# Kernel optimization log

Hardware: AMD Instinct MI355X
Metric: run time of the kernel (lower is better)

The kernel has to match this reference:

```python
import jax, jax.numpy as jnp
import numpy as np

B, L, D = 512, 200, 128
N_ITEMS = 50001
T_STEPS = 4
TAU = 2.0
STEP = 1
V_TH = 1.0
SG_ALPHA = 4.0  # spikingjelly default surrogate.Sigmoid alpha


@jax.custom_vjp
def spike(x):
    return (x >= 0.0).astype(x.dtype)

def _spike_fwd(x):
    return spike(x), x

def _spike_bwd(x, g):
    s = jax.nn.sigmoid(SG_ALPHA * x)
    return (g * SG_ALPHA * s * (1.0 - s),)

spike.defvjp(_spike_fwd, _spike_bwd)


def lif_multistep(x):
    """Multi-step LIF (hard reset to 0, detach_reset). x: [T, ...] -> spikes [T, ...]."""
    def step(v, xt):
        v = v + (xt - v) / TAU  # charge (v_reset = 0)
        s = spike(v - V_TH)
        v = v - jax.lax.stop_gradient(s) * v  # hard reset, detached spike
        return v, s
    v0 = jnp.zeros_like(x[0])
    _, spikes = jax.lax.scan(step, v0, x)
    return spikes


def layernorm(x, g, b, eps=1e-5):
    m = x.mean(-1, keepdims=True)
    v = x.var(-1, keepdims=True)
    return (x - m) / jnp.sqrt(v + eps) * g + b


def _build_session_graphs(rng):
    lens = rng.integers(50, L + 1, size=B)
    item_seq = np.zeros((B, L), dtype=np.int64)
    for b in range(B):
        item_seq[b, :lens[b]] = rng.integers(1, N_ITEMS, size=lens[b])
    alias = np.zeros((B, L), dtype=np.int64)
    items = np.zeros((B, L), dtype=np.int64)
    A = np.zeros((B, L, 2 * L), dtype=np.float32)
    for b in range(B):
        u = item_seq[b]
        node = np.unique(u)  # sorted
        items[b, :len(node)] = node
        alias[b] = np.searchsorted(node, u)
        uA = np.zeros((L, L), dtype=np.float32)
        for i in range(L - 1):
            if u[i + 1] == 0:
                break
            r = np.searchsorted(node, u[i])
            c = np.searchsorted(node, u[i + 1])
            uA[r, c] = 1.0
        sin = uA.sum(0); sin[sin == 0] = 1.0
        sout = uA.sum(1); sout[sout == 0] = 1.0
        A[b, :, :L] = (uA / sin).T          # u_A_in.T
        A[b, :, L:] = ((uA.T / sout)).T     # u_A_out.T
    mask = item_seq > 0
    return A, alias, items, mask, lens.astype(np.int64)


def setup_inputs() -> dict:
    rng = np.random.default_rng(0)
    A, alias, items, mask, lens = _build_session_graphs(rng)
    stdv = 1.0 / np.sqrt(D)
    key = jax.random.key(0)
    ks = jax.random.split(key, 24)
    u = lambda k, shape: jax.random.uniform(k, shape, jnp.float32, -stdv, stdv)
    item_emb = u(ks[0], (N_ITEMS, D)).at[0].set(0.0)  # padding_idx=0
    return {
        "A": jnp.asarray(A),
        "alias_inputs": jnp.asarray(alias),
        "items": jnp.asarray(items),
        "mask": jnp.asarray(mask),
        "item_seq_len": jnp.asarray(lens),
        "item_emb": item_emb,
        "W_in": u(ks[1], (D, D)), "b_in": u(ks[2], (D,)),
        "W_out": u(ks[3], (D, D)), "b_out": u(ks[4], (D,)),
        "w_ih": u(ks[5], (3 * D, 2 * D)), "w_hh": u(ks[6], (3 * D, D)),
        "b_ih": u(ks[7], (3 * D,)), "b_hh": u(ks[8], (3 * D,)),
        "b_iah": u(ks[9], (D,)), "b_ioh": u(ks[10], (D,)),
        "W1": u(ks[11], (D, D)), "W2": u(ks[12], (D, D)),
        "W3": u(ks[13], (1, D)), "Wt": u(ks[14], (D, 2 * D)),
        "g_q": u(ks[15], (D,)), "beta_q": u(ks[16], (D,)),
        "g_sh": u(ks[17], (2 * D,)), "beta_sh": u(ks[18], (2 * D,)),
    }


def _forward(A, alias_inputs, items, mask, item_seq_len, item_emb,
             W_in, b_in, W_out, b_out, w_ih, w_hh, b_ih, b_hh, b_iah, b_ioh,
             W1, W2, W3, Wt, g_q, beta_q, g_sh, beta_sh):
    hidden = item_emb[items]  # [B,L,D]
    for _ in range(STEP):
        ein = hidden @ W_in.T + b_in
        eout = hidden @ W_out.T + b_out
        input_in = jnp.einsum('bij,bjd->bid', A[:, :, :L], ein) + b_iah
        input_out = jnp.einsum('bij,bjd->bid', A[:, :, L:], eout) + b_ioh
        inputs = jnp.concatenate([input_in, input_out], axis=-1)  # [B,L,2D]
        gi = inputs @ w_ih.T + b_ih  # [B,L,3D]
        gh = hidden @ w_hh.T + b_hh
        i_r, i_i, i_n = jnp.split(gi, 3, axis=-1)
        h_r, h_i, h_n = jnp.split(gh, 3, axis=-1)
        r = jax.nn.sigmoid(i_r + h_r)
        z = jax.nn.sigmoid(i_i + h_i)
        n = jnp.tanh(i_n + r * h_n)
        hidden = (1.0 - z) * hidden + z * n
    seq_hidden = jnp.take_along_axis(hidden, alias_inputs[..., None], axis=1)  # [B,L,D]
    ht = jnp.take_along_axis(seq_hidden, (item_seq_len - 1)[:, None, None], axis=1)[:, 0]  # [B,D]
    Qb = (ht @ W1.T)[:, None, :] + seq_hidden @ W2.T  # [B,L,D]
    Q = jnp.broadcast_to(Qb[None], (T_STEPS, B, L, D))
    Qs = lif_multistep(layernorm(Q, g_q, beta_q))
    alpha = Qs @ W3.T  # [T,B,L,1]
    mf = mask.astype(alpha.dtype)
    a = jnp.sum(alpha * seq_hidden[None] * mf[None, :, :, None], axis=2)  # [T,B,D]
    ht_T = jnp.broadcast_to(ht[None], (T_STEPS, B, D))
    sh = jnp.concatenate([a, ht_T], axis=-1)  # [T,B,2D]
    sh = layernorm(lif_multistep(sh), g_sh, beta_sh)
    return (sh @ Wt.T).mean(0)  # [B,D]


def reference(A, alias_inputs, items, mask, item_seq_len, item_emb,
              W_in, b_in, W_out, b_out, w_ih, w_hh, b_ih, b_hh, b_iah, b_ioh,
              W1, W2, W3, Wt, g_q, beta_q, g_sh, beta_sh):
    return _forward(A, alias_inputs, items, mask, item_seq_len, item_emb,
                    W_in, b_in, W_out, b_out, w_ih, w_hh, b_ih, b_hh, b_iah, b_ioh,
                    W1, W2, W3, Wt, g_q, beta_q, g_sh, beta_sh)
```

## Files before the change

kernel.cpp:

```cpp
#include <hip/hip_runtime.h>
#include <hip/hip_bf16.h>
#include <cstdint>
#include <cstddef>

#define B_ 512
#define L_ 200
#define D_ 128
#define M_ (B_*L_)
#define T_ 4

typedef short bf16x8 __attribute__((ext_vector_type(8)));
typedef unsigned short u16x8 __attribute__((ext_vector_type(8)));
typedef float f32x4 __attribute__((ext_vector_type(4)));

__device__ __forceinline__ float bf2f(unsigned short u){
  union { unsigned int i; float f; } c; c.i = ((unsigned int)u)<<16; return c.f;
}
__device__ __forceinline__ unsigned short f2bf(float f){
  union { float f; unsigned int i; } c; c.f = f;
  unsigned int r = c.i + 0x7FFFu + ((c.i>>16)&1u);
  return (unsigned short)(r>>16);
}
__device__ __forceinline__ float wsum(float v){
  #pragma unroll
  for (int m=1;m<64;m<<=1) v += __shfl_xor(v, m, 64);
  return v;
}
__device__ __forceinline__ void gload_lds16(const void* g, void* l){
  __builtin_amdgcn_global_load_lds(
      (const __attribute__((address_space(1))) void*)g,
      (__attribute__((address_space(3))) void*)l, 16, 0, 0);
}

__global__ __launch_bounds__(256)
void gemm_bt(const unsigned short* __restrict__ A, int lda,
             const unsigned short* __restrict__ Bt, int ldb,
             const float* __restrict__ bias,
             unsigned short* __restrict__ C, int ldc, int K,
             const int* __restrict__ mlimit, const int* __restrict__ gidx)
{
  const int m0 = blockIdx.y * 128;
  const int Mv = mlimit ? *mlimit : (1<<30);
  if (m0 >= Mv) return;
  __shared__ __align__(16) short sAs[2][128*32];
  __shared__ __align__(16) short sBs[2][128*32];
  const int tid = threadIdx.x;
  const int n0 = blockIdx.x * 128;
  const int lane = tid & 63;
  const int w = tid >> 6;
  const int wr = (w>>1)*64, wc = (w&1)*64;

  f32x4 acc[4][4];
  #pragma unroll
  for (int i=0;i<4;i++)
    #pragma unroll
    for (int j=0;j<4;j++) acc[i][j] = (f32x4){0.f,0.f,0.f,0.f};

  const int c1 = tid, c2 = tid + 256;
  const int r1 = c1>>2, s1 = c1&3, k1 = ((s1 ^ ((r1>>1)&3))&3)<<3;
  const int r2 = c2>>2, s2 = c2&3, k2 = ((s2 ^ ((r2>>1)&3))&3)<<3;
  int ar1 = m0 + r1, ar2 = m0 + r2;
  if (gidx){ ar1 = (ar1 < Mv) ? gidx[ar1] : 0; ar2 = (ar2 < Mv) ? gidx[ar2] : 0; }
  const int fr = lane & 15;
  const int fq = lane >> 4;
  const int fk = ((fq ^ ((fr>>1)&3))&3)<<3;

  auto stage = [&](int t){
    const int buf = t & 1, ks = t << 5;
    gload_lds16(A  + (size_t)ar1*lda + ks + k1, sAs[buf] + (size_t)c1*8);
    gload_lds16(A  + (size_t)ar2*lda + ks + k2, sAs[buf] + (size_t)c2*8);
    gload_lds16(Bt + (size_t)(n0 + r1)*ldb + ks + k1, sBs[buf] + (size_t)c1*8);
    gload_lds16(Bt + (size_t)(n0 + r2)*ldb + ks + k2, sBs[buf] + (size_t)c2*8);
  };
  const int nT = K >> 5;
  stage(0);
  __syncthreads();
  for (int t=0; t<nT; ++t){
    if (t+1 < nT) stage(t+1);
    const short* a_ = sAs[t&1];
    const short* b_ = sBs[t&1];
    bf16x8 af[4], bfr[4];
    #pragma unroll
    for (int i=0;i<4;i++){
      af[i]  = *(const bf16x8*)(a_ + (wr + i*16 + fr)*32 + fk);
      bfr[i] = *(const bf16x8*)(b_ + (wc + i*16 + fr)*32 + fk);
    }
    #pragma unroll
    for (int i=0;i<4;i++)
      #pragma unroll
      for (int j=0;j<4;j++)
        acc[i][j] = __builtin_amdgcn_mfma_f32_16x16x32_bf16(af[i], bfr[j], acc[i][j], 0,0,0);
    __syncthreads();
  }

  const int orow = fq<<2;
  #pragma unroll
  for (int i=0;i<4;i++){
    #pragma unroll
    for (int j=0;j<4;j++){
      const int gn = n0 + wc + j*16 + fr;
      const float bv = bias ? bias[gn] : 0.f;
      #pragma unroll
      for (int v=0;v<4;v++){
        const int gm = m0 + wr + i*16 + orow + v;
        C[(size_t)gm*ldc + gn] = f2bf(acc[i][j][v] + bv);
      }
    }
  }
}

__global__ __launch_bounds__(128)
void k_prepW(const float* __restrict__ w_ih, const float* __restrict__ w_hh,
             const float* __restrict__ W_in, const float* __restrict__ W_out,
             const float* __restrict__ b_in, const float* __restrict__ b_out,
             const float* __restrict__ b_ih, const float* __restrict__ b_hh,
             const float* __restrict__ b_iah, const float* __restrict__ b_ioh,
             const float* __restrict__ W2,
             unsigned short* __restrict__ Wbig, float* __restrict__ biasBase,
             float* __restrict__ uIn, float* __restrict__ uOut,
             unsigned short* __restrict__ w2b)
{
  const int p = blockIdx.x, t = threadIdx.x;
  if (p < 128) w2b[p*128 + t] = f2bf(W2[p*128 + t]);
  const int dim = p>>2, g = p&3;
  const int row = (g==0) ? dim : (g==1) ? 128+dim : 256+dim;
  const bool has_ih = (g!=3), has_hh = (g!=2);
  __shared__ float wl[128], wrg[128], red[3][128];
  wl[t]  = has_ih ? w_ih[(size_t)row*256 + t]       : 0.f;
  wrg[t] = has_ih ? w_ih[(size_t)row*256 + 128 + t] : 0.f;
  __syncthreads();
  float cin = 0.f, cout = 0.f;
  if (has_ih) {
    for (int m=0;m<128;m++){
      cin  += wl[m]  * W_in [m*128 + t];
      cout += wrg[m] * W_out[m*128 + t];
    }
  }
  Wbig[(size_t)p*384 +       t] = f2bf(cin);
  Wbig[(size_t)p*384 + 128 + t] = f2bf(cout);
  Wbig[(size_t)p*384 + 256 + t] = f2bf(has_hh ? w_hh[(size_t)row*128 + t] : 0.f);
  red[0][t] = wl[t]*b_iah[t] + wrg[t]*b_ioh[t];
  red[1][t] = wl[t]*b_in[t];
  red[2][t] = wrg[t]*b_out[t];
  __syncthreads();
  if (t == 0) {
    float v=0.f, ui=0.f, uo=0.f;
    for (int k=0;k<128;k++){ v += red[0][k]; ui += red[1][k]; uo += red[2][k]; }
    float bb;
    if (g==0)      bb = b_ih[dim]     + b_hh[dim]     + v;
    else if (g==1) bb = b_ih[128+dim] + b_hh[128+dim] + v;
    else if (g==2) bb = b_ih[256+dim] + v;
    else           bb = b_hh[256+dim];
    biasBase[p] = bb;
    uIn[p]  = has_ih ? ui : 0.f;
    uOut[p] = has_ih ? uo : 0.f;
  }
}

__global__ __launch_bounds__(64)
void k_nb(const int* __restrict__ alias, const int* __restrict__ lens,
          int* __restrict__ nb)
{
  const int b = blockIdx.x, lane = threadIdx.x;
  const int len = lens[b];
  int m = 0;
  for (int l=lane; l<len; l+=64) m = max(m, alias[b*L_ + l]);
  #pragma unroll
  for (int o=1;o<64;o<<=1) m = max(m, __shfl_xor(m, o, 64));
  if (lane==0) nb[b] = m + 1;
}

__global__ __launch_bounds__(512)
void k_scan(const int* __restrict__ nb, const int* __restrict__ lens,
            int* __restrict__ nbase, int* __restrict__ vbase)
{
  __shared__ int A[2][512], Bv[2][512];
  const int t = threadIdx.x;
  const int a0 = nb[t], b0 = lens[t];
  A[0][t] = a0; Bv[0][t] = b0;
  __syncthreads();
  int cur = 0;
  for (int off=1; off<512; off<<=1){
    const int nxt = cur^1;
    A[nxt][t]  = A[cur][t]  + (t>=off ? A[cur][t-off]  : 0);
    Bv[nxt][t] = Bv[cur][t] + (t>=off ? Bv[cur][t-off] : 0);
    __syncthreads();
    cur = nxt;
  }
  nbase[t] = A[cur][t] - a0;
  vbase[t] = Bv[cur][t] - b0;
  if (t==511){ nbase[512] = A[cur][511]; vbase[512] = Bv[cur][511]; }
}

__global__ __launch_bounds__(1024)
void k_aggemb(const int* __restrict__ alias, const int* __restrict__ items,
              const int* __restrict__ lens, const float* __restrict__ emb,
              const int* __restrict__ nb, const int* __restrict__ nbase,
              const int* __restrict__ vbase,
              unsigned short* __restrict__ X3, unsigned char* __restrict__ cf,
              int* __restrict__ gidx)
{
  const int b = blockIdx.x, tid = threadIdx.x;
  __shared__ unsigned short hl[L_*128];
  __shared__ int al[L_], it[L_];
  __shared__ unsigned bmIn[L_*8], bmOut[L_*8];
  if (tid < L_) { al[tid] = alias[b*L_ + tid]; it[tid] = items[b*L_ + tid]; }
  for (int i=tid; i<L_*8; i+=1024){ bmIn[i]=0u; bmOut[i]=0u; }
  __syncthreads();
  const int len = lens[b], nB = nb[b], base = nbase[b];
  if (tid < len) gidx[vbase[b] + tid] = base + al[tid];
  if (tid < len-1) {
    const int r = al[tid], c = al[tid+1];
    atomicOr(&bmIn[c*8 + (r>>5)],  1u<<(r&31));
    atomicOr(&bmOut[r*8 + (c>>5)], 1u<<(c&31));
  }
  const int rr = tid>>5, cc = (tid&31)<<2;
  for (int s=0; s<nB; s+=32) {
    const int j = s + rr;
    if (j < nB) {
      const float4 v = *(const float4*)(emb + (size_t)it[j]*128 + cc);
      ushort4 o; o.x=f2bf(v.x); o.y=f2bf(v.y); o.z=f2bf(v.z); o.w=f2bf(v.w);
      *(ushort4*)(hl + j*128 + cc) = o;
      *(ushort4*)(X3 + (size_t)(base + j)*384 + 256 + cc) = o;
    }
  }
  __syncthreads();
  const int g = tid >> 7, d = tid & 127;
  for (int s=0; s<nB; s+=8) {
    const int i = s + g;
    if (i < nB) {
      float si=0.f, so=0.f; int ci=0, co=0;
      #pragma unroll
      for (int wd=0; wd<8; ++wd) {
        unsigned word = bmIn[i*8+wd];
        while (word) { int j = __ffs(word)-1; word &= word-1u;
          si += bf2f(hl[(wd*32+j)*128 + d]); ci++; }
        word = bmOut[i*8+wd];
        while (word) { int j = __ffs(word)-1; word &= word-1u;
          so += bf2f(hl[(wd*32+j)*128 + d]); co++; }
      }
      unsigned short* xr = X3 + (size_t)(base + i)*384;
      xr[d]       = f2bf(si / (float)(ci>0?ci:1));
      xr[128 + d] = f2bf(so / (float)(co>0?co:1));
      if (d == 0) cf[base + i] = (unsigned char)((ci>0?1:0) | (co>0?2:0));
    }
  }
}

__global__ __launch_bounds__(512)
void k_gates_gru(const unsigned short* __restrict__ X3,
                 const unsigned short* __restrict__ Wbig,
                 const float* __restrict__ biasBase,
                 const float* __restrict__ uIn,
                 const float* __restrict__ uOut,
                 const unsigned char* __restrict__ cf,
                 unsigned short* __restrict__ hidden,
                 const int* __restrict__ mlimit)
{
  const int m0 = blockIdx.y * 128;
  if (m0 >= *mlimit) return;
  __shared__ __align__(16) short sA[2][128*32];
  __shared__ __align__(16) short sB[2][256*32];
  const int tid = threadIdx.x;
  const int p0 = blockIdx.x * 256;
  const int lane = tid & 63;
  const int w = tid >> 6;
  const int wr  = (w>>2)*64;
  const int wcp = (w&3)*64;
  const int fr = lane & 15;
  const int fq = lane >> 4;
  const int fk = ((fq ^ ((fr>>1)&3))&3)<<3;

  f32x4 acc[4][4];
  #pragma unroll
  for (int i=0;i<4;i++)
    #pragma unroll
    for (int j=0;j<4;j++) acc[i][j] = (f32x4){0.f,0.f,0.f,0.f};

  const int ra = tid>>2, sa_ = tid&3, ka = ((sa_ ^ ((ra>>1)&3))&3)<<3;
  const int c1 = tid + 512, rb1 = c1>>2, sb1 = c1&3, kb1 = ((sb1 ^ ((rb1>>1)&3))&3)<<3;

  auto stage = [&](int t){
    const int buf = t & 1, ks = t << 5;
    gload_lds16(X3   + (size_t)(m0 + ra )*384 + ks + ka , sA[buf] + (size_t)tid*8);
    gload_lds16(Wbig + (size_t)(p0 + ra )*384 + ks + ka , sB[buf] + (size_t)tid*8);
    gload_lds16(Wbig + (size_t)(p0 + rb1)*384 + ks + kb1, sB[buf] + (size_t)(c1-512)*8 + 512*8);
  };
  stage(0);
  __syncthreads();
  for (int t=0; t<12; ++t){
    if (t < 11) stage(t+1);
    const short* a_ = sA[t&1];
    const short* b_ = sB[t&1];
    bf16x8 af[4], bfr[4];
    #pragma unroll
    for (int i=0;i<4;i++){
      af[i]  = *(const bf16x8*)(a_ + (wr  + i*16 + fr)*32 + fk);
      bfr[i] = *(const bf16x8*)(b_ + (wcp + i*16 + fr)*32 + fk);
    }
    #pragma unroll
    for (int i=0;i<4;i++)
      #pragma unroll
      for (int j=0;j<4;j++)
        acc[i][j] = __builtin_amdgcn_mfma_f32_16x16x32_bf16(af[i], bfr[j], acc[i][j], 0,0,0);
    __syncthreads();
  }

  const bool q0b = (lane & 1), q1b = (lane & 2);
  #pragma unroll
  for (int j=0;j<4;j++){
    const int dim = (p0>>2) + (w&3)*16 + j*4 + ((lane>>2)&3);
    const float4 bb = *(const float4*)(biasBase + dim*4);
    const float4 bi = *(const float4*)(uIn  + dim*4);
    const float4 bo = *(const float4*)(uOut + dim*4);
    #pragma unroll
    for (int i=0;i<4;i++){
      const float a0=acc[i][j][0], a1=acc[i][j][1], a2=acc[i][j][2], a3=acc[i][j][3];
      const float t0=__shfl_xor(a0,1), t1=__shfl_xor(a1,1), t2=__shfl_xor(a2,1), t3=__shfl_xor(a3,1);
      const float s0 = q0b? t1:a0, s1 = q0b? a1:t0, s2 = q0b? t3:a2, s3 = q0b? a3:t2;
      const float u0=__shfl_xor(s0,2), u1=__shfl_xor(s1,2), u2=__shfl_xor(s2,2), u3=__shfl_xor(s3,2);
      float G0 = q1b? u2:s0, G1 = q1b? u3:s1, G2 = q1b? s2:u0, G3 = q1b? s3:u1;
      const int row = m0 + wr + i*16 + fq*4 + (lane&3);
      const unsigned c = cf[row];
      const float fi = (c&1) ? 1.f : 0.f, fo = (c&2) ? 1.f : 0.f;
      G0 += bb.x + fi*bi.x + fo*bo.x;
      G1 += bb.y + fi*bi.y + fo*bo.y;
      G2 += bb.z + fi*bi.z + fo*bo.z;
      G3 += bb.w;
      const float h = bf2f(X3[(size_t)row*384 + 256 + dim]);
      const float r = 1.f/(1.f+__expf(-G0));
      const float z = 1.f/(1.f+__expf(-G1));
      const float x = G2 + r*G3;
      const float n = 1.f - 2.f/(__expf(2.f*x)+1.f);
      hidden[(size_t)row*128 + dim] = f2bf((1.f-z)*h + z*n);
    }
  }
}

__global__ __launch_bounds__(1024)
void k_attn(const unsigned short* __restrict__ Q0,
            const unsigned short* __restrict__ hidden, const int* __restrict__ gidx,
            const int* __restrict__ lens, const int* __restrict__ vbase,
            const float* __restrict__ W1,
            const float* __restrict__ g_q, const float* __restrict__ beta_q,
            const float* __restrict__ W3,
            const float* __restrict__ g_sh, const float* __restrict__ beta_sh,
            const float* __restrict__ Wt, float* __restrict__ out)
{
  const int b = blockIdx.x, tid = threadIdx.x;
  const int w = tid>>6, lane = tid&63;
  __shared__ float a_acc[16][T_][128];
  __shared__ float htv[128], htw[128];
  __shared__ float ys[256];
  __shared__ float part[T_][4];
  const int len = lens[b], vb = vbase[b];
  for (int i=tid; i<16*T_*128; i+=1024) ((float*)a_acc)[i] = 0.f;
  if (tid < 128) htv[tid] = bf2f(hidden[(size_t)gidx[vb + len - 1]*128 + tid]);
  __syncthreads();
  {
    const int d = tid >> 3, seg = (tid & 7) << 4;
    const float* wr1 = W1 + (size_t)d*128 + seg;
    const float* hv = htv + seg;
    float p = 0.f;
    #pragma unroll
    for (int k=0;k<16;k++) p += wr1[k]*hv[k];
    p += __shfl_xor(p, 1, 64); p += __shfl_xor(p, 2, 64); p += __shfl_xor(p, 4, 64);
    if ((tid & 7) == 0) htw[d] = p;
  }
  __syncthreads();
  const float h0 = htw[lane], h1 = htw[lane+64];
  const float gq0 = g_q[lane], gq1 = g_q[lane+64];
  const float bq0 = beta_q[lane], bq1 = beta_q[lane+64];
  const float w30 = W3[lane], w31 = W3[lane+64];
  for (int l = w; l < len; l += 16) {
    const size_t row = (size_t)(vb + l);
    const size_t hrow = (size_t)gidx[row];
    const float q0 = bf2f(Q0[row*128 + lane]) + h0;
    const float q1 = bf2f(Q0[row*128 + lane + 64]) + h1;
    const float m = wsum(q0+q1) * (1.f/128.f);
    const float d0 = q0-m, d1 = q1-m;
    const float var = wsum(d0*d0 + d1*d1) * (1.f/128.f);
    const float inv = rsqrtf(var + 1e-5f);
    const float x0 = d0*inv*gq0 + bq0;
    const float x1 = d1*inv*gq1 + bq1;
    const float sh0 = bf2f(hidden[hrow*128+lane]), sh1 = bf2f(hidden[hrow*128+lane+64]);
    float v0=0.f, v1=0.f;
    #pragma unroll
    for (int t=0;t<T_;t++){
      v0 = 0.5f*(v0+x0); v1 = 0.5f*(v1+x1);
      const float s0 = (v0>=1.f)?1.f:0.f, s1 = (v1>=1.f)?1.f:0.f;
      v0 -= s0*v0; v1 -= s1*v1;
      const float alpha = wsum(s0*w30 + s1*w31);
      a_acc[w][t][lane] += alpha*sh0; a_acc[w][t][lane+64] += alpha*sh1;
    }
  }
  __syncthreads();

  float sp[T_] = {0.f,0.f,0.f,0.f};
  if (tid < 256) {
    const float xh = (tid >= 128) ? htv[tid-128] : 0.f;
    float v = 0.f;
    #pragma unroll
    for (int t=0;t<T_;t++){
      float x;
      if (tid < 128) {
        x = 0.f;
        #pragma unroll
        for (int p=0;p<16;p++) x += a_acc[p][t][tid];
      } else x = xh;
      v = 0.5f*(v + x);
      const float s = (v>=1.f)?1.f:0.f;
      v -= s*v;
      sp[t] = s;
    }
    #pragma unroll
    for (int t=0;t<T_;t++){
      const float r = wsum(sp[t]);
      if (lane==0) part[t][w] = r;
    }
  }
  __syncthreads();
  if (tid < 256) {
    float acc4 = 0.f;
    #pragma unroll
    for (int t=0;t<T_;t++){
      const float k = part[t][0]+part[t][1]+part[t][2]+part[t][3];
      const float mean = k * (1.f/256.f);
      const float varr = mean - mean*mean;
      const float inv = rsqrtf(varr + 1e-5f);
      acc4 += (sp[t]-mean)*inv;
    }
    ys[tid] = acc4*g_sh[tid] + 4.f*beta_sh[tid];
  }
  __syncthreads();
  if (tid < 128) {
    float acc = 0.f;
    const float4* wr4 = (const float4*)(Wt + (size_t)tid*256);
    const float4* ys4 = (const float4*)ys;
    #pragma unroll 8
    for (int k=0;k<64;k++){
      const float4 wv = wr4[k], yv = ys4[k];
      acc += wv.x*yv.x + wv.y*yv.y + wv.z*yv.z + wv.w*yv.w;
    }
    out[(size_t)b*128 + tid] = acc*0.25f;
  }
}

extern "C" void kernel_launch(void* const* d_in, const int* in_sizes, int n_in,
                              void* d_out, int out_size, void* d_ws, size_t ws_size,
                              hipStream_t stream)
{
  const int*   alias  = (const int*)d_in[1];
  const int*   items  = (const int*)d_in[2];
  const int*   lens   = (const int*)d_in[4];
  const float* emb    = (const float*)d_in[5];
  const float* W_in   = (const float*)d_in[6];
  const float* b_in   = (const float*)d_in[7];
  const float* W_out  = (const float*)d_in[8];
  const float* b_out  = (const float*)d_in[9];
  const float* w_ih   = (const float*)d_in[10];
  const float* w_hh   = (const float*)d_in[11];
  const float* b_ih   = (const float*)d_in[12];
  const float* b_hh   = (const float*)d_in[13];
  const float* b_iah  = (const float*)d_in[14];
  const float* b_ioh  = (const float*)d_in[15];
  const float* W1     = (const float*)d_in[16];
  const float* W2     = (const float*)d_in[17];
  const float* W3     = (const float*)d_in[18];
  const float* Wt     = (const float*)d_in[19];
  const float* g_q    = (const float*)d_in[20];
  const float* beta_q = (const float*)d_in[21];
  const float* g_sh   = (const float*)d_in[22];
  const float* beta_sh= (const float*)d_in[23];

  char* ws = (char*)d_ws;
  size_t off = 0;
  auto alloc = [&](size_t bytes)->void* {
    void* p = ws + off; off += (bytes + 255) & ~(size_t)255; return p;
  };
  unsigned short* X3    = (unsigned short*)alloc((size_t)M_*384*2);
  unsigned short* hidden= (unsigned short*)alloc((size_t)M_*128*2);
  unsigned short* Q0c   = (unsigned short*)alloc((size_t)M_*128*2);
  int*            gidx  = (int*)alloc((size_t)M_*4);
  unsigned short* Wbig  = (unsigned short*)alloc((size_t)512*384*2);
  unsigned short* w2b   = (unsigned short*)alloc(16384*2);
  float*          biasBase = (float*)alloc(512*4);
  float*          uIn   = (float*)alloc(512*4);
  float*          uOut  = (float*)alloc(512*4);
  unsigned char*  cf    = (unsigned char*)alloc(M_);
  int*            nb    = (int*)alloc(512*4);
  int*            nbase = (int*)alloc(513*4);
  int*            vbase = (int*)alloc(513*4);
  if (off > ws_size) return;

  k_prepW<<<512,128,0,stream>>>(w_ih,w_hh,W_in,W_out,b_in,b_out,b_ih,b_hh,
                                b_iah,b_ioh,W2,Wbig,biasBase,uIn,uOut,w2b);
  k_nb<<<B_,64,0,stream>>>(alias, lens, nb);
  k_scan<<<1,512,0,stream>>>(nb, lens, nbase, vbase);
  k_aggemb<<<B_,1024,0,stream>>>(alias, items, lens, emb, nb, nbase, vbase,
                                 X3, cf, gidx);
  k_gates_gru<<<dim3(2,800),512,0,stream>>>(X3, Wbig, biasBase, uIn, uOut, cf,
                                            hidden, nbase+512);
  gemm_bt<<<dim3(1,800),256,0,stream>>>(hidden, 128, w2b, 128, nullptr, Q0c, 128,
                                        128, vbase+512, gidx);
  k_attn<<<B_,1024,0,stream>>>(Q0c, hidden, gidx, lens, vbase, W1, g_q, beta_q,
                               W3, g_sh, beta_sh, Wt, (float*)d_out);
}
```

Before: 180.0 us.

## Fuse GRU gate kernel with W2 projection and merge node-count into prepW

Each GRU block now covers all 512 gate columns for its 128 rows, keeps the new hidden tile in LDS, and runs the W2 projection there, writing Q0 per unique node rather than per sequence position. The separate gather GEMM and the k_nb kernel are dropped, and k_attn indexes Q0 through gidx. This removes a kernel launch, a re-read of hidden and redundant Q0 work for repeated items. In exchange each block uses much more LDS and more accumulator registers (4x8 tiles), which lowers occupancy, and the grid falls from 1600 to 800 blocks.

```diff
diff --git a/kernel.cpp b/kernel.cpp
--- a/kernel.cpp
+++ b/kernel.cpp
@@ -30,83 +30,6 @@
   __builtin_amdgcn_global_load_lds(
       (const __attribute__((address_space(1))) void*)g,
       (__attribute__((address_space(3))) void*)l, 16, 0, 0);
-}
-
-__global__ __launch_bounds__(256)
-void gemm_bt(const unsigned short* __restrict__ A, int lda,
-             const unsigned short* __restrict__ Bt, int ldb,
-             const float* __restrict__ bias,
-             unsigned short* __restrict__ C, int ldc, int K,
-             const int* __restrict__ mlimit, const int* __restrict__ gidx)
-{
-  const int m0 = blockIdx.y * 128;
-  const int Mv = mlimit ? *mlimit : (1<<30);
-  if (m0 >= Mv) return;
-  __shared__ __align__(16) short sAs[2][128*32];
-  __shared__ __align__(16) short sBs[2][128*32];
-  const int tid = threadIdx.x;
-  const int n0 = blockIdx.x * 128;
-  const int lane = tid & 63;
-  const int w = tid >> 6;
-  const int wr = (w>>1)*64, wc = (w&1)*64;
-
-  f32x4 acc[4][4];
-  #pragma unroll
-  for (int i=0;i<4;i++)
-    #pragma unroll
-    for (int j=0;j<4;j++) acc[i][j] = (f32x4){0.f,0.f,0.f,0.f};
-
-  const int c1 = tid, c2 = tid + 256;
-  const int r1 = c1>>2, s1 = c1&3, k1 = ((s1 ^ ((r1>>1)&3))&3)<<3;
-  const int r2 = c2>>2, s2 = c2&3, k2 = ((s2 ^ ((r2>>1)&3))&3)<<3;
-  int ar1 = m0 + r1, ar2 = m0 + r2;
-  if (gidx){ ar1 = (ar1 < Mv) ? gidx[ar1] : 0; ar2 = (ar2 < Mv) ? gidx[ar2] : 0; }
-  const int fr = lane & 15;
-  const int fq = lane >> 4;
-  const int fk = ((fq ^ ((fr>>1)&3))&3)<<3;
-
-  auto stage = [&](int t){
-    const int buf = t & 1, ks = t << 5;
-    gload_lds16(A  + (size_t)ar1*lda + ks + k1, sAs[buf] + (size_t)c1*8);
-    gload_lds16(A  + (size_t)ar2*lda + ks + k2, sAs[buf] + (size_t)c2*8);
-    gload_lds16(Bt + (size_t)(n0 + r1)*ldb + ks + k1, sBs[buf] + (size_t)c1*8);
-    gload_lds16(Bt + (size_t)(n0 + r2)*ldb + ks + k2, sBs[buf] + (size_t)c2*8);
-  };
-  const int nT = K >> 5;
-  stage(0);
-  __syncthreads();
-  for (int t=0; t<nT; ++t){
-    if (t+1 < nT) stage(t+1);
-    const short* a_ = sAs[t&1];
-    const short* b_ = sBs[t&1];
-    bf16x8 af[4], bfr[4];
-    #pragma unroll
-    for (int i=0;i<4;i++){
-      af[i]  = *(const bf16x8*)(a_ + (wr + i*16 + fr)*32 + fk);
-      bfr[i] = *(const bf16x8*)(b_ + (wc + i*16 + fr)*32 + fk);
-    }
-    #pragma unroll
-    for (int i=0;i<4;i++)
-      #pragma unroll
-      for (int j=0;j<4;j++)
-        acc[i][j] = __builtin_amdgcn_mfma_f32_16x16x32_bf16(af[i], bfr[j], acc[i][j], 0,0,0);
-    __syncthreads();
-  }
-
-  const int orow = fq<<2;
-  #pragma unroll
-  for (int i=0;i<4;i++){
-    #pragma unroll
-    for (int j=0;j<4;j++){
-      const int gn = n0 + wc + j*16 + fr;
-      const float bv = bias ? bias[gn] : 0.f;
-      #pragma unroll
-      for (int v=0;v<4;v++){
-        const int gm = m0 + wr + i*16 + orow + v;
-        C[(size_t)gm*ldc + gn] = f2bf(acc[i][j][v] + bv);
-      }
-    }
-  }
 }
 
 __global__ __launch_bounds__(128)
@@ -116,9 +39,10 @@
              const float* __restrict__ b_ih, const float* __restrict__ b_hh,
              const float* __restrict__ b_iah, const float* __restrict__ b_ioh,
              const float* __restrict__ W2,
+             const int* __restrict__ alias, const int* __restrict__ lens,
              unsigned short* __restrict__ Wbig, float* __restrict__ biasBase,
              float* __restrict__ uIn, float* __restrict__ uOut,
-             unsigned short* __restrict__ w2b)
+             unsigned short* __restrict__ w2b, int* __restrict__ nb)
 {
   const int p = blockIdx.x, t = threadIdx.x;
   if (p < 128) w2b[p*128 + t] = f2bf(W2[p*128 + t]);
@@ -155,19 +79,14 @@
     uIn[p]  = has_ih ? ui : 0.f;
     uOut[p] = has_ih ? uo : 0.f;
   }
-}
-
-__global__ __launch_bounds__(64)
-void k_nb(const int* __restrict__ alias, const int* __restrict__ lens,
-          int* __restrict__ nb)
-{
-  const int b = blockIdx.x, lane = threadIdx.x;
-  const int len = lens[b];
-  int m = 0;
-  for (int l=lane; l<len; l+=64) m = max(m, alias[b*L_ + l]);
-  #pragma unroll
-  for (int o=1;o<64;o<<=1) m = max(m, __shfl_xor(m, o, 64));
-  if (lane==0) nb[b] = m + 1;
+  if (t < 64) {
+    const int len = lens[p];
+    int m = 0;
+    for (int l=t; l<len; l+=64) m = max(m, alias[p*L_ + l]);
+    #pragma unroll
+    for (int o=1;o<64;o<<=1) m = max(m, __shfl_xor(m, o, 64));
+    if (t==0) nb[p] = m + 1;
+  }
 }
 
 __global__ __launch_bounds__(512)
@@ -248,43 +167,49 @@
 }
 
 __global__ __launch_bounds__(512)
-void k_gates_gru(const unsigned short* __restrict__ X3,
-                 const unsigned short* __restrict__ Wbig,
-                 const float* __restrict__ biasBase,
-                 const float* __restrict__ uIn,
-                 const float* __restrict__ uOut,
-                 const unsigned char* __restrict__ cf,
-                 unsigned short* __restrict__ hidden,
-                 const int* __restrict__ mlimit)
-{
-  const int m0 = blockIdx.y * 128;
+void k_gates_q0(const unsigned short* __restrict__ X3,
+                const unsigned short* __restrict__ Wbig,
+                const unsigned short* __restrict__ w2b,
+                const float* __restrict__ biasBase,
+                const float* __restrict__ uIn,
+                const float* __restrict__ uOut,
+                const unsigned char* __restrict__ cf,
+                unsigned short* __restrict__ hidden,
+                unsigned short* __restrict__ q0n,
+                const int* __restrict__ mlimit)
+{
+  const int m0 = blockIdx.x * 128;
   if (m0 >= *mlimit) return;
   __shared__ __align__(16) short sA[2][128*32];
-  __shared__ __align__(16) short sB[2][256*32];
+  __shared__ __align__(16) short sB[2][512*32];
   const int tid = threadIdx.x;
-  const int p0 = blockIdx.x * 256;
   const int lane = tid & 63;
   const int w = tid >> 6;
   const int wr  = (w>>2)*64;
-  const int wcp = (w&3)*64;
+  const int wcp = (w&3)*128;
   const int fr = lane & 15;
   const int fq = lane >> 4;
   const int fk = ((fq ^ ((fr>>1)&3))&3)<<3;
 
-  f32x4 acc[4][4];
+  f32x4 acc[4][8];
   #pragma unroll
   for (int i=0;i<4;i++)
     #pragma unroll
-    for (int j=0;j<4;j++) acc[i][j] = (f32x4){0.f,0.f,0.f,0.f};
-
-  const int ra = tid>>2, sa_ = tid&3, ka = ((sa_ ^ ((ra>>1)&3))&3)<<3;
-  const int c1 = tid + 512, rb1 = c1>>2, sb1 = c1&3, kb1 = ((sb1 ^ ((rb1>>1)&3))&3)<<3;
+    for (int j=0;j<8;j++) acc[i][j] = (f32x4){0.f,0.f,0.f,0.f};
+
+  const int rA = tid>>2, sAx = tid&3;
+  const int kA = ((sAx ^ ((rA>>1)&3))&3)<<3;
 
   auto stage = [&](int t){
     const int buf = t & 1, ks = t << 5;
-    gload_lds16(X3   + (size_t)(m0 + ra )*384 + ks + ka , sA[buf] + (size_t)tid*8);
-    gload_lds16(Wbig + (size_t)(p0 + ra )*384 + ks + ka , sB[buf] + (size_t)tid*8);
-    gload_lds16(Wbig + (size_t)(p0 + rb1)*384 + ks + kb1, sB[buf] + (size_t)(c1-512)*8 + 512*8);
+    gload_lds16(X3 + (size_t)(m0 + rA)*384 + ks + kA, sA[buf] + (size_t)tid*8);
+    #pragma unroll
+    for (int q=0;q<4;q++){
+      const int cB = tid + q*512;
+      const int rB = cB>>2, sBx = cB&3;
+      const int kB = ((sBx ^ ((rB>>1)&3))&3)<<3;
+      gload_lds16(Wbig + (size_t)rB*384 + ks + kB, sB[buf] + (size_t)cB*8);
+    }
   };
   stage(0);
   __syncthreads();
@@ -292,24 +217,35 @@
     if (t < 11) stage(t+1);
     const short* a_ = sA[t&1];
     const short* b_ = sB[t&1];
-    bf16x8 af[4], bfr[4];
-    #pragma unroll
-    for (int i=0;i<4;i++){
+    bf16x8 af[4], bfr[8];
+    #pragma unroll
+    for (int i=0;i<4;i++)
       af[i]  = *(const bf16x8*)(a_ + (wr  + i*16 + fr)*32 + fk);
-      bfr[i] = *(const bf16x8*)(b_ + (wcp + i*16 + fr)*32 + fk);
-    }
+    #pragma unroll
+    for (int j=0;j<8;j++)
+      bfr[j] = *(const bf16x8*)(b_ + (wcp + j*16 + fr)*32 + fk);
     #pragma unroll
     for (int i=0;i<4;i++)
       #pragma unroll
-      for (int j=0;j<4;j++)
+      for (int j=0;j<8;j++)
         acc[i][j] = __builtin_amdgcn_mfma_f32_16x16x32_bf16(af[i], bfr[j], acc[i][j], 0,0,0);
     __syncthreads();
   }
 
+  short* hl  = sB[0];
+  short* w2l = sB[1];
+
+  #pragma unroll
+  for (int q=0;q<4;q++){
+    const int cW = tid + q*512;
+    const int rW = cW>>4, sW = cW&15;
+    gload_lds16(w2b + (size_t)rW*128 + ((sW ^ (rW&7))<<3), w2l + (size_t)cW*8);
+  }
+
   const bool q0b = (lane & 1), q1b = (lane & 2);
   #pragma unroll
-  for (int j=0;j<4;j++){
-    const int dim = (p0>>2) + (w&3)*16 + j*4 + ((lane>>2)&3);
+  for (int j=0;j<8;j++){
+    const int dim = (w&3)*32 + j*4 + ((lane>>2)&3);
     const float4 bb = *(const float4*)(biasBase + dim*4);
     const float4 bi = *(const float4*)(uIn  + dim*4);
     const float4 bo = *(const float4*)(uOut + dim*4);
@@ -332,13 +268,53 @@
       const float z = 1.f/(1.f+__expf(-G1));
       const float x = G2 + r*G3;
       const float n = 1.f - 2.f/(__expf(2.f*x)+1.f);
-      hidden[(size_t)row*128 + dim] = f2bf((1.f-z)*h + z*n);
+      const unsigned short hv = f2bf((1.f-z)*h + z*n);
+      hidden[(size_t)row*128 + dim] = hv;
+      const int rl = row - m0;
+      hl[rl*128 + (((dim>>3) ^ (rl&7))<<3) + (dim&7)] = hv;
+    }
+  }
+  __syncthreads();
+
+  f32x4 acc2[4][2];
+  #pragma unroll
+  for (int i=0;i<4;i++){ acc2[i][0]=(f32x4){0,0,0,0}; acc2[i][1]=(f32x4){0,0,0,0}; }
+  const int wc2 = (w&3)*32;
+  #pragma unroll
+  for (int kk=0;kk<4;kk++){
+    bf16x8 af2[4], bf2_[2];
+    #pragma unroll
+    for (int i=0;i<4;i++){
+      const int r = wr + i*16 + fr;
+      af2[i] = *(const bf16x8*)(hl + r*128 + (((kk*4 + fq) ^ (r&7))<<3));
+    }
+    #pragma unroll
+    for (int j=0;j<2;j++){
+      const int c = wc2 + j*16 + fr;
+      bf2_[j] = *(const bf16x8*)(w2l + c*128 + (((kk*4 + fq) ^ (c&7))<<3));
+    }
+    #pragma unroll
+    for (int i=0;i<4;i++)
+      #pragma unroll
+      for (int j=0;j<2;j++)
+        acc2[i][j] = __builtin_amdgcn_mfma_f32_16x16x32_bf16(af2[i], bf2_[j], acc2[i][j], 0,0,0);
+  }
+  #pragma unroll
+  for (int i=0;i<4;i++){
+    #pragma unroll
+    for (int j=0;j<2;j++){
+      const int col = wc2 + j*16 + fr;
+      #pragma unroll
+      for (int v=0;v<4;v++){
+        const int row = m0 + wr + i*16 + fq*4 + v;
+        q0n[(size_t)row*128 + col] = f2bf(acc2[i][j][v]);
+      }
     }
   }
 }
 
 __global__ __launch_bounds__(1024)
-void k_attn(const unsigned short* __restrict__ Q0,
+void k_attn(const unsigned short* __restrict__ q0n,
             const unsigned short* __restrict__ hidden, const int* __restrict__ gidx,
             const int* __restrict__ lens, const int* __restrict__ vbase,
             const float* __restrict__ W1,
@@ -375,8 +351,8 @@
   for (int l = w; l < len; l += 16) {
     const size_t row = (size_t)(vb + l);
     const size_t hrow = (size_t)gidx[row];
-    const float q0 = bf2f(Q0[row*128 + lane]) + h0;
-    const float q1 = bf2f(Q0[row*128 + lane + 64]) + h1;
+    const float q0 = bf2f(q0n[hrow*128 + lane]) + h0;
+    const float q1 = bf2f(q0n[hrow*128 + lane + 64]) + h1;
     const float m = wsum(q0+q1) * (1.f/128.f);
     const float d0 = q0-m, d1 = q1-m;
     const float var = wsum(d0*d0 + d1*d1) * (1.f/128.f);
@@ -480,7 +456,7 @@
   };
   unsigned short* X3    = (unsigned short*)alloc((size_t)M_*384*2);
   unsigned short* hidden= (unsigned short*)alloc((size_t)M_*128*2);
-  unsigned short* Q0c   = (unsigned short*)alloc((size_t)M_*128*2);
+  unsigned short* q0n   = (unsigned short*)alloc((size_t)M_*128*2);
   int*            gidx  = (int*)alloc((size_t)M_*4);
   unsigned short* Wbig  = (unsigned short*)alloc((size_t)512*384*2);
   unsigned short* w2b   = (unsigned short*)alloc(16384*2);
@@ -494,15 +470,13 @@
   if (off > ws_size) return;
 
   k_prepW<<<512,128,0,stream>>>(w_ih,w_hh,W_in,W_out,b_in,b_out,b_ih,b_hh,
-                                b_iah,b_ioh,W2,Wbig,biasBase,uIn,uOut,w2b);
-  k_nb<<<B_,64,0,stream>>>(alias, lens, nb);
+                                b_iah,b_ioh,W2,alias,lens,
+                                Wbig,biasBase,uIn,uOut,w2b,nb);
   k_scan<<<1,512,0,stream>>>(nb, lens, nbase, vbase);
   k_aggemb<<<B_,1024,0,stream>>>(alias, items, lens, emb, nb, nbase, vbase,
                                  X3, cf, gidx);
-  k_gates_gru<<<dim3(2,800),512,0,stream>>>(X3, Wbig, biasBase, uIn, uOut, cf,
-                                            hidden, nbase+512);
-  gemm_bt<<<dim3(1,800),256,0,stream>>>(hidden, 128, w2b, 128, nullptr, Q0c, 128,
-                                        128, vbase+512, gidx);
-  k_attn<<<B_,1024,0,stream>>>(Q0c, hidden, gidx, lens, vbase, W1, g_q, beta_q,
+  k_gates_q0<<<800,512,0,stream>>>(X3, Wbig, w2b, biasBase, uIn, uOut, cf,
+                                   hidden, q0n, nbase+512);
+  k_attn<<<B_,1024,0,stream>>>(q0n, hidden, gidx, lens, vbase, W1, g_q, beta_q,
                                W3, g_sh, beta_sh, Wt, (float*)d_out);
 }
```

Measured after the change: 203.2 us. +12.9%, slower.
